# Performance work log

Hardware: AMD Instinct MI355X
Metric: run time of the kernel (lower is better)

## Reference

```python
import jax, jax.numpy as jnp
import numpy as np

B, TQ, TV, DQ, DV, UNITS = 4, 512, 1024, 256, 256, 64


def setup_inputs() -> dict:
    key = jax.random.key(0)
    k1, k2, k3, k4, k5 = jax.random.split(key, 5)
    return {
        "query": jax.random.normal(k1, (B, TQ, DQ), dtype=jnp.float32),
        "value": jax.random.normal(k2, (B, TV, DV), dtype=jnp.float32),
        "w1": jax.random.normal(k3, (DQ, UNITS), dtype=jnp.float32) / np.sqrt(DQ),
        "w2": jax.random.normal(k4, (DV, UNITS), dtype=jnp.float32) / np.sqrt(DV),
        "scale": jax.random.normal(k5, (UNITS,), dtype=jnp.float32),
    }


def reference(query, value, w1, w2, scale):
    # Dense projections (no bias)
    q = jnp.einsum('bqd,du->bqu', query, w1)   # [B,Tq,U]
    k = jnp.einsum('bvd,du->bvu', value, w2)   # [B,Tv,U]
    # Keras AdditiveAttention (use_scale=True):
    # scores[b,q,v] = sum_u scale[u] * tanh(q[b,q,u] + k[b,v,u])
    scores = jnp.einsum('bqvu,u->bqv',
                        jnp.tanh(q[:, :, None, :] + k[:, None, :, :]), scale)
    attn = jax.nn.softmax(scores, axis=-1)      # [B,Tq,Tv]
    context = jnp.einsum('bqv,bvd->bqd', attn, value)  # [B,Tq,Dv]
    return context, attn
```

## Files before the change

kernel.cpp:

```cpp
#include <hip/hip_runtime.h>
#include <math.h>

#define B 4
#define TQ 512
#define TV 1024
#define DQ 256
#define DV 256
#define UNITS 64
#define NQROW (B * TQ)
#define NKROW (B * TV)

#define CEXP  2.885390081777927f
#define LOG2E 1.4426950408889634f

__device__ __forceinline__ float fast_exp2(float x) {
#if __has_builtin(__builtin_amdgcn_exp2f)
    return __builtin_amdgcn_exp2f(x);
#else
    return __expf(0.6931471805599453f * x);
#endif
}

__device__ __forceinline__ float wave_sum(float v) {
    #pragma unroll
    for (int off = 32; off > 0; off >>= 1)
        v += __shfl_xor(v, off, 64);
    return v;
}

__device__ __forceinline__ unsigned short f2bf(float f) {
    unsigned int b = __float_as_uint(f);
    return (unsigned short)((b + 0x7fffu + ((b >> 16) & 1u)) >> 16);
}

#define RPB 8
__global__ __launch_bounds__(256) void proj_kernel(
        const float* __restrict__ query, const float* __restrict__ value,
        const float* __restrict__ w1, const float* __restrict__ w2,
        float* __restrict__ Eq, float* __restrict__ EkT,
        unsigned short* __restrict__ vbf) {
    __shared__ float rows[RPB][DQ];
    __shared__ float part[4][RPB][UNITS + 2];
    const int tid = threadIdx.x;
    const int u   = tid & 63;
    const int wid = tid >> 6;
    const int row0 = blockIdx.x * RPB;
    const bool isq = row0 < NQROW;
    const float* in = isq ? query + (size_t)row0 * DQ
                          : value + (size_t)(row0 - NQROW) * DQ;
    const float* w  = isq ? w1 : w2;

    {
        const float4* src = (const float4*)in;
        float4* dst = (float4*)&rows[0][0];
        dst[tid]       = src[tid];
        dst[tid + 256] = src[tid + 256];
    }
    __syncthreads();

    float a[RPB] = {};
    const int c0 = wid * 16;
    #pragma unroll 4
    for (int ci = 0; ci < 16; ++ci) {
        const int c = c0 + ci;
        const float w0v = w[(4 * c + 0) * UNITS + u];
        const float w1v = w[(4 * c + 1) * UNITS + u];
        const float w2v = w[(4 * c + 2) * UNITS + u];
        const float w3v = w[(4 * c + 3) * UNITS + u];
        #pragma unroll
        for (int r = 0; r < RPB; ++r) {
            const float4 t = *(const float4*)&rows[r][4 * c];
            a[r] = fmaf(t.x, w0v, a[r]);
            a[r] = fmaf(t.y, w1v, a[r]);
            a[r] = fmaf(t.z, w2v, a[r]);
            a[r] = fmaf(t.w, w3v, a[r]);
        }
    }
    #pragma unroll
    for (int r = 0; r < RPB; ++r)
        part[wid][r][u] = a[r];
    __syncthreads();

    if (isq) {
        #pragma unroll
        for (int h = 0; h < 2; ++h) {
            const int p = tid + h * 256;
            const int row = p >> 6, uu = p & 63;
            const float s = (part[0][row][uu] + part[1][row][uu]) +
                            (part[2][row][uu] + part[3][row][uu]);
            Eq[(size_t)(row0 + row) * UNITS + uu] = fast_exp2(CEXP * s);
        }
    } else {
        #pragma unroll
        for (int h = 0; h < 2; ++h) {
            const int p = tid + h * 256;
            const int uu = p >> 3, r = p & 7;
            const float s = (part[0][r][uu] + part[1][r][uu]) +
                            (part[2][r][uu] + part[3][r][uu]);
            EkT[(size_t)uu * NKROW + (row0 - NQROW) + r] = fast_exp2(CEXP * s);
        }
        const float* rf = &rows[0][0];
        const int base = tid * 8;
        uint4 pk;
        pk.x = (unsigned)f2bf(rf[base + 0]) | ((unsigned)f2bf(rf[base + 1]) << 16);
        pk.y = (unsigned)f2bf(rf[base + 2]) | ((unsigned)f2bf(rf[base + 3]) << 16);
        pk.z = (unsigned)f2bf(rf[base + 4]) | ((unsigned)f2bf(rf[base + 5]) << 16);
        pk.w = (unsigned)f2bf(rf[base + 6]) | ((unsigned)f2bf(rf[base + 7]) << 16);
        *(uint4*)(vbf + (size_t)(row0 - NQROW) * DV + base) = pk;
    }
}

#define QB 4
#define SNW 4
__global__ __launch_bounds__(256) void sc_kernel(
        const float* __restrict__ Eq,
        const float* __restrict__ EkT,
        const float* __restrict__ scale,
        const unsigned short* __restrict__ vbf,
        float* __restrict__ out_attn,
        float* __restrict__ out_ctx) {
    __shared__ float a_lds[QB][TV];
    __shared__ float q_lds[QB][UNITS];
    __shared__ float s_lds[UNITS];
    __shared__ float reds[QB][SNW];

    const int tid = threadIdx.x, lane = tid & 63, wid = tid >> 6;
    int bid = blockIdx.x;
    bid = (bid & 7) * ((NQROW / QB) >> 3) + (bid >> 3);
    const int b  = bid / (TQ / QB);
    const int q0 = (bid % (TQ / QB)) * QB;

    if (tid < QB * UNITS)
        q_lds[tid >> 6][tid & 63] =
            Eq[(size_t)(b * TQ + q0 + (tid >> 6)) * UNITS + (tid & 63)];
    __syncthreads();
    if (tid < UNITS) s_lds[tid] = scale[tid];
    __syncthreads();

    const float* ekc = EkT + (size_t)b * TV + 4 * tid;
    float4 acc[QB];
    #pragma unroll
    for (int q = 0; q < QB; ++q) { acc[q].x = acc[q].y = acc[q].z = acc[q].w = 0.f; }

    #pragma unroll 2
    for (int u4 = 0; u4 < UNITS / 4; ++u4) {
        const float4 ekA = *(const float4*)(ekc + (size_t)(4 * u4 + 0) * NKROW);
        const float4 ekB = *(const float4*)(ekc + (size_t)(4 * u4 + 1) * NKROW);
        const float4 ekC = *(const float4*)(ekc + (size_t)(4 * u4 + 2) * NKROW);
        const float4 ekD = *(const float4*)(ekc + (size_t)(4 * u4 + 3) * NKROW);
        const float4 s4 = *(const float4*)(s_lds + 4 * u4);
        #pragma unroll
        for (int q = 0; q < QB; ++q) {
            const float4 eq = *(const float4*)(&q_lds[q][4 * u4]);
            #define EVAL(comp)                                                   \
            {                                                                    \
                float t0 = fmaf(eq.x, ekA.comp, 1.f);                            \
                float t1 = fmaf(eq.y, ekB.comp, 1.f);                            \
                float t2 = fmaf(eq.z, ekC.comp, 1.f);                            \
                float t3 = fmaf(eq.w, ekD.comp, 1.f);                            \
                float p01 = t0 * t1, p23 = t2 * t3;                              \
                float A  = fmaf(s4.y, t0, s4.x * t1);                            \
                float Bq = fmaf(s4.w, t2, s4.z * t3);                            \
                float num = fmaf(Bq, p01, A * p23);                              \
                float r = __builtin_amdgcn_rcpf(p01 * p23);                      \
                acc[q].comp = fmaf(num, r, acc[q].comp);                         \
            }
            EVAL(x) EVAL(y) EVAL(z) EVAL(w)
            #undef EVAL
        }
    }

    float4 e[QB];
    #pragma unroll
    for (int q = 0; q < QB; ++q) {
        e[q].x = fast_exp2(-2.f * LOG2E * acc[q].x);
        e[q].y = fast_exp2(-2.f * LOG2E * acc[q].y);
        e[q].z = fast_exp2(-2.f * LOG2E * acc[q].z);
        e[q].w = fast_exp2(-2.f * LOG2E * acc[q].w);
        float s = wave_sum((e[q].x + e[q].y) + (e[q].z + e[q].w));
        if (lane == 0) reds[q][wid] = s;
    }
    __syncthreads();
    #pragma unroll
    for (int q = 0; q < QB; ++q) {
        float ss = (reds[q][0] + reds[q][1]) + (reds[q][2] + reds[q][3]);
        const float inv = __builtin_amdgcn_rcpf(ss);
        float4 o;
        o.x = e[q].x * inv; o.y = e[q].y * inv;
        o.z = e[q].z * inv; o.w = e[q].w * inv;
        *(float4*)(&a_lds[q][4 * tid]) = o;
        *(float4*)(out_attn + (size_t)(b * TQ + q0 + q) * TV + 4 * tid) = o;
    }
    __syncthreads();

    const int vq = tid >> 6;
    const int dp = tid & 63;
    const int d0 = dp * 4;
    const unsigned short* vb = vbf + ((size_t)b * TV + vq * 256) * DV + d0;
    float4 c[QB];
    #pragma unroll
    for (int q = 0; q < QB; ++q) { c[q].x = c[q].y = c[q].z = c[q].w = 0.f; }

    #pragma unroll 2
    for (int v4 = 0; v4 < 64; ++v4) {
        const int v = vq * 256 + v4 * 4;
        const float4 a0 = *(const float4*)&a_lds[0][v];
        const float4 a1 = *(const float4*)&a_lds[1][v];
        const float4 a2 = *(const float4*)&a_lds[2][v];
        const float4 a3 = *(const float4*)&a_lds[3][v];
        #define STEP(j, comp)                                                    \
        {                                                                        \
            const ushort4 wv = *(const ushort4*)(vb + (size_t)(v4 * 4 + j) * DV);\
            const float v0 = __uint_as_float((unsigned)wv.x << 16);              \
            const float v1 = __uint_as_float((unsigned)wv.y << 16);              \
            const float v2 = __uint_as_float((unsigned)wv.z << 16);              \
            const float v3 = __uint_as_float((unsigned)wv.w << 16);              \
            c[0].x = fmaf(a0.comp, v0, c[0].x); c[0].y = fmaf(a0.comp, v1, c[0].y); \
            c[0].z = fmaf(a0.comp, v2, c[0].z); c[0].w = fmaf(a0.comp, v3, c[0].w); \
            c[1].x = fmaf(a1.comp, v0, c[1].x); c[1].y = fmaf(a1.comp, v1, c[1].y); \
            c[1].z = fmaf(a1.comp, v2, c[1].z); c[1].w = fmaf(a1.comp, v3, c[1].w); \
            c[2].x = fmaf(a2.comp, v0, c[2].x); c[2].y = fmaf(a2.comp, v1, c[2].y); \
            c[2].z = fmaf(a2.comp, v2, c[2].z); c[2].w = fmaf(a2.comp, v3, c[2].w); \
            c[3].x = fmaf(a3.comp, v0, c[3].x); c[3].y = fmaf(a3.comp, v1, c[3].y); \
            c[3].z = fmaf(a3.comp, v2, c[3].z); c[3].w = fmaf(a3.comp, v3, c[3].w); \
        }
        STEP(0, x) STEP(1, y) STEP(2, z) STEP(3, w)
        #undef STEP
    }
    __syncthreads();

    float* red = &a_lds[0][0];
    if (vq != 0) {
        float* r = red + (((vq - 1) * QB) * 64 + dp) * 4;
        #pragma unroll
        for (int q = 0; q < QB; ++q)
            *(float4*)(r + q * 64 * 4) = c[q];
    }
    __syncthreads();
    if (vq == 0) {
        #pragma unroll
        for (int g = 0; g < 3; ++g) {
            const float* r = red + ((g * QB) * 64 + dp) * 4;
            #pragma unroll
            for (int q = 0; q < QB; ++q) {
                const float4 t = *(const float4*)(r + q * 64 * 4);
                c[q].x += t.x; c[q].y += t.y; c[q].z += t.z; c[q].w += t.w;
            }
        }
        #pragma unroll
        for (int q = 0; q < QB; ++q)
            *(float4*)(out_ctx + (size_t)(b * TQ + q0 + q) * DV + d0) = c[q];
    }
}

extern "C" void kernel_launch(void* const* d_in, const int* in_sizes, int n_in,
                              void* d_out, int out_size, void* d_ws, size_t ws_size,
                              hipStream_t stream) {
    const float* query = (const float*)d_in[0];
    const float* value = (const float*)d_in[1];
    const float* w1    = (const float*)d_in[2];
    const float* w2    = (const float*)d_in[3];
    const float* scale = (const float*)d_in[4];

    float* out      = (float*)d_out;
    float* out_ctx  = out;
    float* out_attn = out + (size_t)NQROW * DV;

    float* Eq  = (float*)d_ws;
    float* EkT = Eq + (size_t)NQROW * UNITS;
    unsigned short* vbf = (unsigned short*)(EkT + (size_t)UNITS * NKROW);

    proj_kernel<<<dim3((NQROW + NKROW) / RPB), 256, 0, stream>>>(
        query, value, w1, w2, Eq, EkT, vbf);
    sc_kernel<<<dim3(NQROW / QB), 256, 0, stream>>>(
        Eq, EkT, scale, vbf, out_attn, out_ctx);
}
```

Baseline: 49.60 us.

## Double sc_kernel block size and split units and value dims across wave halves

The score kernel now runs 512 threads per block. The two halves of the block each reduce 32 of the 64 units, and their partial sums are combined through LDS before the softmax. The context accumulation is split across 8 wave groups of 128 values each, with a 7-way LDS reduction at the end. The aim is more waves per block and shorter dependent loops, at the cost of extra LDS traffic, barriers, larger shared memory, and half the threads sitting idle during the softmax.

```diff
diff --git a/kernel.cpp b/kernel.cpp
--- a/kernel.cpp
+++ b/kernel.cpp
@@ -111,18 +111,20 @@
 }
 
 #define QB 4
-#define SNW 4
-__global__ __launch_bounds__(256) void sc_kernel(
+__global__ __launch_bounds__(512) void sc_kernel(
         const float* __restrict__ Eq,
         const float* __restrict__ EkT,
         const float* __restrict__ scale,
         const unsigned short* __restrict__ vbf,
         float* __restrict__ out_attn,
         float* __restrict__ out_ctx) {
-    __shared__ float a_lds[QB][TV];
+    __shared__ float pool[QB * TV + 256 * QB * 4];
     __shared__ float q_lds[QB][UNITS];
     __shared__ float s_lds[UNITS];
-    __shared__ float reds[QB][SNW];
+    __shared__ float reds[QB][4];
+
+    float* a_lds = pool;
+    float4* scr  = (float4*)(pool + QB * TV);
 
     const int tid = threadIdx.x, lane = tid & 63, wid = tid >> 6;
     int bid = blockIdx.x;
@@ -133,25 +135,28 @@
     if (tid < QB * UNITS)
         q_lds[tid >> 6][tid & 63] =
             Eq[(size_t)(b * TQ + q0 + (tid >> 6)) * UNITS + (tid & 63)];
-    __syncthreads();
-    if (tid < UNITS) s_lds[tid] = scale[tid];
-    __syncthreads();
-
-    const float* ekc = EkT + (size_t)b * TV + 4 * tid;
+    else if (tid < QB * UNITS + UNITS)
+        s_lds[tid - QB * UNITS] = scale[tid - QB * UNITS];
+    __syncthreads();
+
+    const int uh = tid >> 8;
+    const int vt = tid & 255;
+    const int ub = uh * 32;
+    const float* ekc = EkT + (size_t)b * TV + 4 * vt + (size_t)ub * NKROW;
     float4 acc[QB];
     #pragma unroll
     for (int q = 0; q < QB; ++q) { acc[q].x = acc[q].y = acc[q].z = acc[q].w = 0.f; }
 
     #pragma unroll 2
-    for (int u4 = 0; u4 < UNITS / 4; ++u4) {
+    for (int u4 = 0; u4 < 8; ++u4) {
         const float4 ekA = *(const float4*)(ekc + (size_t)(4 * u4 + 0) * NKROW);
         const float4 ekB = *(const float4*)(ekc + (size_t)(4 * u4 + 1) * NKROW);
         const float4 ekC = *(const float4*)(ekc + (size_t)(4 * u4 + 2) * NKROW);
         const float4 ekD = *(const float4*)(ekc + (size_t)(4 * u4 + 3) * NKROW);
-        const float4 s4 = *(const float4*)(s_lds + 4 * u4);
+        const float4 s4 = *(const float4*)(s_lds + ub + 4 * u4);
         #pragma unroll
         for (int q = 0; q < QB; ++q) {
-            const float4 eq = *(const float4*)(&q_lds[q][4 * u4]);
+            const float4 eq = *(const float4*)(&q_lds[q][ub + 4 * u4]);
             #define EVAL(comp)                                                   \
             {                                                                    \
                 float t0 = fmaf(eq.x, ekA.comp, 1.f);                            \
@@ -170,44 +175,57 @@
         }
     }
 
+    if (uh) {
+        #pragma unroll
+        for (int q = 0; q < QB; ++q)
+            scr[vt * QB + q] = acc[q];
+    }
+    __syncthreads();
+
     float4 e[QB];
-    #pragma unroll
-    for (int q = 0; q < QB; ++q) {
-        e[q].x = fast_exp2(-2.f * LOG2E * acc[q].x);
-        e[q].y = fast_exp2(-2.f * LOG2E * acc[q].y);
-        e[q].z = fast_exp2(-2.f * LOG2E * acc[q].z);
-        e[q].w = fast_exp2(-2.f * LOG2E * acc[q].w);
-        float s = wave_sum((e[q].x + e[q].y) + (e[q].z + e[q].w));
-        if (lane == 0) reds[q][wid] = s;
-    }
-    __syncthreads();
-    #pragma unroll
-    for (int q = 0; q < QB; ++q) {
-        float ss = (reds[q][0] + reds[q][1]) + (reds[q][2] + reds[q][3]);
-        const float inv = __builtin_amdgcn_rcpf(ss);
-        float4 o;
-        o.x = e[q].x * inv; o.y = e[q].y * inv;
-        o.z = e[q].z * inv; o.w = e[q].w * inv;
-        *(float4*)(&a_lds[q][4 * tid]) = o;
-        *(float4*)(out_attn + (size_t)(b * TQ + q0 + q) * TV + 4 * tid) = o;
+    if (!uh) {
+        #pragma unroll
+        for (int q = 0; q < QB; ++q) {
+            const float4 t = scr[vt * QB + q];
+            acc[q].x += t.x; acc[q].y += t.y; acc[q].z += t.z; acc[q].w += t.w;
+            e[q].x = fast_exp2(-2.f * LOG2E * acc[q].x);
+            e[q].y = fast_exp2(-2.f * LOG2E * acc[q].y);
+            e[q].z = fast_exp2(-2.f * LOG2E * acc[q].z);
+            e[q].w = fast_exp2(-2.f * LOG2E * acc[q].w);
+            float s = wave_sum((e[q].x + e[q].y) + (e[q].z + e[q].w));
+            if (lane == 0) reds[q][wid] = s;
+        }
+    }
+    __syncthreads();
+    if (!uh) {
+        #pragma unroll
+        for (int q = 0; q < QB; ++q) {
+            const float ss = (reds[q][0] + reds[q][1]) + (reds[q][2] + reds[q][3]);
+            const float inv = __builtin_amdgcn_rcpf(ss);
+            float4 o;
+            o.x = e[q].x * inv; o.y = e[q].y * inv;
+            o.z = e[q].z * inv; o.w = e[q].w * inv;
+            *(float4*)(a_lds + q * TV + 4 * vt) = o;
+            *(float4*)(out_attn + (size_t)(b * TQ + q0 + q) * TV + 4 * vt) = o;
+        }
     }
     __syncthreads();
 
     const int vq = tid >> 6;
     const int dp = tid & 63;
     const int d0 = dp * 4;
-    const unsigned short* vb = vbf + ((size_t)b * TV + vq * 256) * DV + d0;
+    const unsigned short* vb = vbf + ((size_t)b * TV + vq * 128) * DV + d0;
     float4 c[QB];
     #pragma unroll
     for (int q = 0; q < QB; ++q) { c[q].x = c[q].y = c[q].z = c[q].w = 0.f; }
 
     #pragma unroll 2
-    for (int v4 = 0; v4 < 64; ++v4) {
-        const int v = vq * 256 + v4 * 4;
-        const float4 a0 = *(const float4*)&a_lds[0][v];
-        const float4 a1 = *(const float4*)&a_lds[1][v];
-        const float4 a2 = *(const float4*)&a_lds[2][v];
-        const float4 a3 = *(const float4*)&a_lds[3][v];
+    for (int v4 = 0; v4 < 32; ++v4) {
+        const int v = vq * 128 + v4 * 4;
+        const float4 a0 = *(const float4*)(a_lds + 0 * TV + v);
+        const float4 a1 = *(const float4*)(a_lds + 1 * TV + v);
+        const float4 a2 = *(const float4*)(a_lds + 2 * TV + v);
+        const float4 a3 = *(const float4*)(a_lds + 3 * TV + v);
         #define STEP(j, comp)                                                    \
         {                                                                        \
             const ushort4 wv = *(const ushort4*)(vb + (size_t)(v4 * 4 + j) * DV);\
@@ -229,9 +247,8 @@
     }
     __syncthreads();
 
-    float* red = &a_lds[0][0];
     if (vq != 0) {
-        float* r = red + (((vq - 1) * QB) * 64 + dp) * 4;
+        float* r = pool + (size_t)(vq - 1) * (QB * 64 * 4) + (0 * 64 + dp) * 4;
         #pragma unroll
         for (int q = 0; q < QB; ++q)
             *(float4*)(r + q * 64 * 4) = c[q];
@@ -239,8 +256,8 @@
     __syncthreads();
     if (vq == 0) {
         #pragma unroll
-        for (int g = 0; g < 3; ++g) {
-            const float* r = red + ((g * QB) * 64 + dp) * 4;
+        for (int g = 0; g < 7; ++g) {
+            const float* r = pool + (size_t)g * (QB * 64 * 4) + dp * 4;
             #pragma unroll
             for (int q = 0; q < QB; ++q) {
                 const float4 t = *(const float4*)(r + q * 64 * 4);
@@ -272,6 +289,6 @@
 
     proj_kernel<<<dim3((NQROW + NKROW) / RPB), 256, 0, stream>>>(
         query, value, w1, w2, Eq, EkT, vbf);
-    sc_kernel<<<dim3(NQROW / QB), 256, 0, stream>>>(
+    sc_kernel<<<dim3(NQROW / QB), 512, 0, stream>>>(
         Eq, EkT, scale, vbf, out_attn, out_ctx);
 }
```

Measured after the change: 43.46 us. 1.14x faster.
